# Optimization experiments

Measured on AMD Instinct MI355X. Metric: run time of the kernel, lower is better.

## Reference

```python
import jax, jax.numpy as jnp
import numpy as np

N = 100000   # nodes
DEG = 16     # fixed neighbor count per node
F_IN = 128
F_OUT = 32
H = 4        # heads


def setup_inputs() -> dict:
    key = jax.random.key(0)
    k1, k2, k3, k4 = jax.random.split(key, 4)
    x = jax.random.normal(k1, (N, F_IN), dtype=jnp.float32)
    neigh_idx = jax.random.randint(k2, (N, DEG), 0, N)
    # small scale keeps exp(leaky_relu(score)) well-conditioned (original exp's pre-softmax)
    Ws = jax.random.normal(k3, (H, F_OUT, F_IN), dtype=jnp.float32) * 0.05
    As = jax.random.normal(k4, (H, 2 * F_OUT, 1), dtype=jnp.float32) * 0.05
    return {"x": x, "neigh_idx": neigh_idx, "Ws": Ws, "As": As}


def reference(x, neigh_idx, Ws, As):
    n, _ = x.shape
    h, f_out, _ = Ws.shape
    # transformed node features per head: [H, N, F_out]
    t = jnp.einsum('hoi,ni->hno', Ws, x)
    # score a^T [Wh_src; Wh_dst] decomposes into src + dst dot products
    a = As[..., 0]                      # [H, 2*F_out]
    a_src, a_dst = a[:, :f_out], a[:, f_out:]
    s_src = jnp.einsum('hno,ho->hn', t, a_src)   # [H, N]
    s_dst = jnp.einsum('hno,ho->hn', t, a_dst)   # [H, N]
    # self node goes first in the softmax, matching the original loop
    full_idx = jnp.concatenate([jnp.arange(n)[:, None], neigh_idx], axis=1)  # [N, DEG+1]
    scores = s_src[:, :, None] + s_dst[:, full_idx]                           # [H, N, DEG+1]
    # faithful to original: exp(leaky_relu(.)) THEN softmax (double exponential)
    e = jnp.exp(jax.nn.leaky_relu(scores, 0.2))
    alphas = jax.nn.softmax(e, axis=-1)
    feats = t[:, full_idx]                                                    # [H, N, DEG+1, F_out]
    out = jnp.einsum('hnd,hndf->hnf', alphas, feats)                          # [H, N, F_out]
    # activation 'elu' -> heads concatenated: [N, H*F_out]
    out = jnp.transpose(out, (1, 0, 2)).reshape(n, h * f_out)
    return jax.nn.elu(out)
```

## Files before the change

### kernel.cpp

```cpp
#include <hip/hip_runtime.h>
#include <hip/hip_fp16.h>
#include <math.h>

#define NN 100000
#define DEG 16
#define F_IN 128
#define F_OUT 32
#define NH 4
#define FTOT 128

#define BM 128
#define BK 32
#define PAD 132

__global__ __launch_bounds__(256) void k1_proj(
    const float* __restrict__ x,
    const float* __restrict__ W,
    const float* __restrict__ As,
    __half* __restrict__ t,
    float* __restrict__ ssrc,
    float* __restrict__ sdst) {
    __shared__ float xs[2][BK][PAD];
    __shared__ float ws_[2][BK][PAD];

    const int tid = threadIdx.x;
    const int base = blockIdx.x * BM;

    float4 rx[4], rw[4];

    auto load_chunk = [&](int k0) {
#pragma unroll
        for (int r = 0; r < 4; ++r) {
            const int q = tid + 256 * r;
            const int n = q >> 3;
            const int c = q & 7;
            int ng = base + n;
            if (ng >= NN) ng = NN - 1;
            rx[r] = *(const float4*)(x + (long)ng * F_IN + k0 + 4 * c);
            rw[r] = *(const float4*)(W + n * F_IN + k0 + 4 * c);
        }
    };
    auto write_chunk = [&](int buf) {
#pragma unroll
        for (int r = 0; r < 4; ++r) {
            const int q = tid + 256 * r;
            const int n = q >> 3;
            const int c = q & 7;
            xs[buf][4 * c + 0][n] = rx[r].x;
            xs[buf][4 * c + 1][n] = rx[r].y;
            xs[buf][4 * c + 2][n] = rx[r].z;
            xs[buf][4 * c + 3][n] = rx[r].w;
            ws_[buf][4 * c + 0][n] = rw[r].x;
            ws_[buf][4 * c + 1][n] = rw[r].y;
            ws_[buf][4 * c + 2][n] = rw[r].z;
            ws_[buf][4 * c + 3][n] = rw[r].w;
        }
    };

    load_chunk(0);
    write_chunk(0);
    __syncthreads();
    load_chunk(32);

    const int lane = tid & 63;
    const int wv = tid >> 6;
    const int wr = wv >> 1;
    const int wc = wv & 1;
    const int ln = lane & 7;
    const int lf = lane >> 3;
    const int nq0 = wr * 64 + ln * 8;
    const int fq0 = wc * 64 + lf * 8;

    float acc[8][8];
#pragma unroll
    for (int j = 0; j < 8; ++j)
#pragma unroll
        for (int q = 0; q < 8; ++q) acc[j][q] = 0.f;

    for (int ch = 0; ch < 4; ++ch) {
        const int buf = ch & 1;
#pragma unroll 8
        for (int kk = 0; kk < BK; ++kk) {
            const float4 xa = *(const float4*)&xs[buf][kk][nq0];
            const float4 xb = *(const float4*)&xs[buf][kk][nq0 + 4];
            const float4 wa = *(const float4*)&ws_[buf][kk][fq0];
            const float4 wb = *(const float4*)&ws_[buf][kk][fq0 + 4];
            const float xn[8] = {xa.x, xa.y, xa.z, xa.w, xb.x, xb.y, xb.z, xb.w};
            const float wf[8] = {wa.x, wa.y, wa.z, wa.w, wb.x, wb.y, wb.z, wb.w};
#pragma unroll
            for (int j = 0; j < 8; ++j)
#pragma unroll
                for (int q = 0; q < 8; ++q) acc[j][q] += xn[j] * wf[q];
        }
        if (ch < 3) {
            __syncthreads();
            write_chunk(buf ^ 1);
            __syncthreads();
            if (ch < 2) load_chunk(32 * (ch + 2));
        }
    }

#pragma unroll
    for (int j = 0; j < 8; ++j) {
        const int n = base + nq0 + j;
        if (n < NN) {
            union { __half h[8]; float4 v; } u;
#pragma unroll
            for (int q = 0; q < 8; ++q) u.h[q] = __float2half_rn(acc[j][q]);
            *(float4*)(t + (long)n * FTOT + fq0) = u.v;
        }
    }

    const int h = wc * 2 + (lf >> 2);
    const int o0 = (lf & 3) * 8;
    const float4 a0 = *(const float4*)(As + h * 64 + o0);
    const float4 a1 = *(const float4*)(As + h * 64 + o0 + 4);
    const float4 b0 = *(const float4*)(As + h * 64 + 32 + o0);
    const float4 b1 = *(const float4*)(As + h * 64 + 32 + o0 + 4);
    const float av[8] = {a0.x, a0.y, a0.z, a0.w, a1.x, a1.y, a1.z, a1.w};
    const float bv[8] = {b0.x, b0.y, b0.z, b0.w, b1.x, b1.y, b1.z, b1.w};
#pragma unroll
    for (int j = 0; j < 8; ++j) {
        float ps = 0.f, pd = 0.f;
#pragma unroll
        for (int q = 0; q < 8; ++q) {
            ps += acc[j][q] * av[q];
            pd += acc[j][q] * bv[q];
        }
        ps += __shfl_xor(ps, 8);  ps += __shfl_xor(ps, 16);
        pd += __shfl_xor(pd, 8);  pd += __shfl_xor(pd, 16);
        if ((lf & 3) == 0) {
            const int n = base + nq0 + j;
            if (n < NN) {
                ssrc[(long)n * NH + h] = ps;
                sdst[(long)n * NH + h] = pd;
            }
        }
    }
}

__global__ __launch_bounds__(256) void k2_attn(
    const int* __restrict__ nidx,
    const __half* __restrict__ t,
    const float* __restrict__ ssrc,
    const float* __restrict__ sdst,
    float* __restrict__ out) {
    __shared__ float salpha[4][17][4];
    __shared__ int sidx[4][17];

    const int lane = threadIdx.x & 63;
    const int wv = threadIdx.x >> 6;
    const int n = blockIdx.x * 4 + wv;

    if (lane < 17) {
        sidx[wv][lane] = (lane == 0) ? n : nidx[(long)n * DEG + (lane - 1)];
    }
    __syncthreads();

    unsigned int pre[17];
#pragma unroll
    for (int d = 0; d < 17; ++d) {
        pre[d] = *(const unsigned int*)(t + (long)sidx[wv][d] * FTOT + 2 * lane);
    }

    const int h = lane >> 4;
    const int j = lane & 15;
    const float ssv = ssrc[(long)n * NH + h];

    float e_a;
    {
        float c = ssv + sdst[(long)sidx[wv][j] * NH + h];
        c = fmaxf(c, 0.f) + 0.2f * fminf(c, 0.f);
        e_a = expf(c);
    }
    float e_b = -INFINITY;
    if (j == 15) {
        float c = ssv + sdst[(long)sidx[wv][16] * NH + h];
        c = fmaxf(c, 0.f) + 0.2f * fminf(c, 0.f);
        e_b = expf(c);
    }

    float m = fmaxf(e_a, e_b);
#pragma unroll
    for (int mask = 8; mask >= 1; mask >>= 1)
        m = fmaxf(m, __shfl_xor(m, mask));

    const float pa = expf(e_a - m);
    const float pb = (j == 15) ? expf(e_b - m) : 0.f;
    float s = pa + pb;
#pragma unroll
    for (int mask = 8; mask >= 1; mask >>= 1)
        s += __shfl_xor(s, mask);

    const float inv = 1.0f / s;
    salpha[wv][j][h] = pa * inv;
    if (j == 15) salpha[wv][16][h] = pb * inv;
    __syncthreads();

    const int hc = lane >> 4;
    float ax = 0.f, ay = 0.f;
#pragma unroll
    for (int d = 0; d < 17; ++d) {
        const float a = salpha[wv][d][hc];
        const float2 f = __half22float2(*(const __half2*)&pre[d]);
        ax += a * f.x;
        ay += a * f.y;
    }

    const float yx = ax > 0.f ? ax : expm1f(ax);
    const float yy = ay > 0.f ? ay : expm1f(ay);
    float2 o = make_float2(yx, yy);
    *(float2*)(out + (long)n * FTOT + 2 * lane) = o;
}

extern "C" void kernel_launch(void* const* d_in, const int* in_sizes, int n_in,
                              void* d_out, int out_size, void* d_ws, size_t ws_size,
                              hipStream_t stream) {
    const float* x = (const float*)d_in[0];
    const int* nidx = (const int*)d_in[1];
    const float* W = (const float*)d_in[2];
    const float* As = (const float*)d_in[3];
    float* out = (float*)d_out;

    __half* t = (__half*)d_ws;
    float* ssrc = (float*)((char*)d_ws + (size_t)NN * FTOT * sizeof(__half));
    float* sdst = ssrc + (size_t)NN * NH;

    k1_proj<<<(NN + BM - 1) / BM, 256, 0, stream>>>(x, W, As, t, ssrc, sdst);
    k2_attn<<<NN / 4, 256, 0, stream>>>(nidx, t, ssrc, sdst, out);
}
```

Measured before the change: 219.5 us.

## Rewrite projection GEMM with fp16 MFMA and swizzled LDS; nontemporal loads/stores in attention

The projection kernel drops the fp32 register-tiled FMA GEMM. It converts x and W to fp16 in swizzled shared memory and computes the product with 16x16x32 f16 MFMA instructions, using 64-node tiles. The output tile is staged through LDS for coalesced fp16 stores, and the attention scores are reduced with lane shuffles. The attention kernel switches to nontemporal loads for neighbor indices and nontemporal stores for the output. Rounding x and W to fp16 before the matmul loses input precision, and the whole of W is reloaded per block.

```diff
diff --git a/kernel.cpp b/kernel.cpp
--- a/kernel.cpp
+++ b/kernel.cpp
@@ -9,9 +9,12 @@
 #define NH 4
 #define FTOT 128
 
-#define BM 128
-#define BK 32
-#define PAD 132
+typedef _Float16 f16x8 __attribute__((ext_vector_type(8)));
+typedef float f32x4 __attribute__((ext_vector_type(4)));
+
+__device__ __forceinline__ int swz(int row, int col) {
+    return row * 128 + (col ^ ((row & 7) << 3));
+}
 
 __global__ __launch_bounds__(256) void k1_proj(
     const float* __restrict__ x,
@@ -20,120 +23,114 @@
     __half* __restrict__ t,
     float* __restrict__ ssrc,
     float* __restrict__ sdst) {
-    __shared__ float xs[2][BK][PAD];
-    __shared__ float ws_[2][BK][PAD];
+    __shared__ __half xs[64 * 128];
+    __shared__ __half wsh[128 * 128];
 
     const int tid = threadIdx.x;
-    const int base = blockIdx.x * BM;
-
-    float4 rx[4], rw[4];
-
-    auto load_chunk = [&](int k0) {
-#pragma unroll
-        for (int r = 0; r < 4; ++r) {
-            const int q = tid + 256 * r;
-            const int n = q >> 3;
-            const int c = q & 7;
-            int ng = base + n;
-            if (ng >= NN) ng = NN - 1;
-            rx[r] = *(const float4*)(x + (long)ng * F_IN + k0 + 4 * c);
-            rw[r] = *(const float4*)(W + n * F_IN + k0 + 4 * c);
-        }
-    };
-    auto write_chunk = [&](int buf) {
-#pragma unroll
-        for (int r = 0; r < 4; ++r) {
-            const int q = tid + 256 * r;
-            const int n = q >> 3;
-            const int c = q & 7;
-            xs[buf][4 * c + 0][n] = rx[r].x;
-            xs[buf][4 * c + 1][n] = rx[r].y;
-            xs[buf][4 * c + 2][n] = rx[r].z;
-            xs[buf][4 * c + 3][n] = rx[r].w;
-            ws_[buf][4 * c + 0][n] = rw[r].x;
-            ws_[buf][4 * c + 1][n] = rw[r].y;
-            ws_[buf][4 * c + 2][n] = rw[r].z;
-            ws_[buf][4 * c + 3][n] = rw[r].w;
-        }
-    };
-
-    load_chunk(0);
-    write_chunk(0);
+    const int base = blockIdx.x * 64;
+
+    {
+        const int row = tid >> 2;
+        const int q = tid & 3;
+        int ng = base + row;
+        if (ng >= NN) ng = NN - 1;
+        const float* src = x + (long)ng * F_IN + q * 32;
+#pragma unroll
+        for (int i = 0; i < 4; ++i) {
+            const float4 v0 = *(const float4*)(src + i * 8);
+            const float4 v1 = *(const float4*)(src + i * 8 + 4);
+            union { __half2 h2[4]; float4 f; } u;
+            u.h2[0] = __float22half2_rn(make_float2(v0.x, v0.y));
+            u.h2[1] = __float22half2_rn(make_float2(v0.z, v0.w));
+            u.h2[2] = __float22half2_rn(make_float2(v1.x, v1.y));
+            u.h2[3] = __float22half2_rn(make_float2(v1.z, v1.w));
+            *(float4*)&xs[swz(row, q * 32 + i * 8)] = u.f;
+        }
+    }
+    {
+        const int row = tid >> 1;
+        const int hq = tid & 1;
+        const float* src = W + row * F_IN + hq * 64;
+#pragma unroll
+        for (int i = 0; i < 8; ++i) {
+            const float4 v0 = *(const float4*)(src + i * 8);
+            const float4 v1 = *(const float4*)(src + i * 8 + 4);
+            union { __half2 h2[4]; float4 f; } u;
+            u.h2[0] = __float22half2_rn(make_float2(v0.x, v0.y));
+            u.h2[1] = __float22half2_rn(make_float2(v0.z, v0.w));
+            u.h2[2] = __float22half2_rn(make_float2(v1.x, v1.y));
+            u.h2[3] = __float22half2_rn(make_float2(v1.z, v1.w));
+            *(float4*)&wsh[swz(row, hq * 64 + i * 8)] = u.f;
+        }
+    }
     __syncthreads();
-    load_chunk(32);
 
     const int lane = tid & 63;
     const int wv = tid >> 6;
-    const int wr = wv >> 1;
-    const int wc = wv & 1;
-    const int ln = lane & 7;
-    const int lf = lane >> 3;
-    const int nq0 = wr * 64 + ln * 8;
-    const int fq0 = wc * 64 + lf * 8;
-
-    float acc[8][8];
-#pragma unroll
-    for (int j = 0; j < 8; ++j)
-#pragma unroll
-        for (int q = 0; q < 8; ++q) acc[j][q] = 0.f;
-
-    for (int ch = 0; ch < 4; ++ch) {
-        const int buf = ch & 1;
-#pragma unroll 8
-        for (int kk = 0; kk < BK; ++kk) {
-            const float4 xa = *(const float4*)&xs[buf][kk][nq0];
-            const float4 xb = *(const float4*)&xs[buf][kk][nq0 + 4];
-            const float4 wa = *(const float4*)&ws_[buf][kk][fq0];
-            const float4 wb = *(const float4*)&ws_[buf][kk][fq0 + 4];
-            const float xn[8] = {xa.x, xa.y, xa.z, xa.w, xb.x, xb.y, xb.z, xb.w};
-            const float wf[8] = {wa.x, wa.y, wa.z, wa.w, wb.x, wb.y, wb.z, wb.w};
-#pragma unroll
-            for (int j = 0; j < 8; ++j)
-#pragma unroll
-                for (int q = 0; q < 8; ++q) acc[j][q] += xn[j] * wf[q];
-        }
-        if (ch < 3) {
-            __syncthreads();
-            write_chunk(buf ^ 1);
-            __syncthreads();
-            if (ch < 2) load_chunk(32 * (ch + 2));
-        }
-    }
-
-#pragma unroll
-    for (int j = 0; j < 8; ++j) {
-        const int n = base + nq0 + j;
+    const int mb = wv * 16;
+    const int lr = lane & 15;
+    const int lg = lane >> 4;
+
+    f16x8 afr[4];
+#pragma unroll
+    for (int kk = 0; kk < 4; ++kk)
+        afr[kk] = *(const f16x8*)&xs[swz(mb + lr, kk * 32 + lg * 8)];
+
+    f32x4 acc[8];
+#pragma unroll
+    for (int nt = 0; nt < 8; ++nt) {
+        f32x4 c = {0.f, 0.f, 0.f, 0.f};
+#pragma unroll
+        for (int kk = 0; kk < 4; ++kk) {
+            const f16x8 b =
+                *(const f16x8*)&wsh[swz(nt * 16 + lr, kk * 32 + lg * 8)];
+            c = __builtin_amdgcn_mfma_f32_16x16x32_f16(afr[kk], b, c, 0, 0, 0);
+        }
+        acc[nt] = c;
+    }
+
+    __half* tst = &xs[mb * 128];
+#pragma unroll
+    for (int nt = 0; nt < 8; ++nt) {
+#pragma unroll
+        for (int r = 0; r < 4; ++r) {
+            const int node = lg * 4 + r;
+            const int feat = nt * 16 + lr;
+            tst[node * 128 + (feat ^ ((node & 7) << 3))] =
+                __float2half_rn(acc[nt][r]);
+        }
+    }
+#pragma unroll
+    for (int r = 0; r < 4; ++r) {
+        const int row = r * 4 + lg;
+        const int n = base + mb + row;
         if (n < NN) {
-            union { __half h[8]; float4 v; } u;
-#pragma unroll
-            for (int q = 0; q < 8; ++q) u.h[q] = __float2half_rn(acc[j][q]);
-            *(float4*)(t + (long)n * FTOT + fq0) = u.v;
-        }
-    }
-
-    const int h = wc * 2 + (lf >> 2);
-    const int o0 = (lf & 3) * 8;
-    const float4 a0 = *(const float4*)(As + h * 64 + o0);
-    const float4 a1 = *(const float4*)(As + h * 64 + o0 + 4);
-    const float4 b0 = *(const float4*)(As + h * 64 + 32 + o0);
-    const float4 b1 = *(const float4*)(As + h * 64 + 32 + o0 + 4);
-    const float av[8] = {a0.x, a0.y, a0.z, a0.w, a1.x, a1.y, a1.z, a1.w};
-    const float bv[8] = {b0.x, b0.y, b0.z, b0.w, b1.x, b1.y, b1.z, b1.w};
-#pragma unroll
-    for (int j = 0; j < 8; ++j) {
-        float ps = 0.f, pd = 0.f;
-#pragma unroll
-        for (int q = 0; q < 8; ++q) {
-            ps += acc[j][q] * av[q];
-            pd += acc[j][q] * bv[q];
-        }
-        ps += __shfl_xor(ps, 8);  ps += __shfl_xor(ps, 16);
-        pd += __shfl_xor(pd, 8);  pd += __shfl_xor(pd, 16);
-        if ((lf & 3) == 0) {
-            const int n = base + nq0 + j;
-            if (n < NN) {
-                ssrc[(long)n * NH + h] = ps;
-                sdst[(long)n * NH + h] = pd;
+            const float4 v =
+                *(const float4*)&tst[row * 128 + ((lr * 8) ^ ((row & 7) << 3))];
+            *(float4*)(t + (long)n * FTOT + lr * 8) = v;
+        }
+    }
+
+#pragma unroll
+    for (int h = 0; h < NH; ++h) {
+        const float as0 = As[h * 64 + lr];
+        const float as1 = As[h * 64 + 16 + lr];
+        const float ad0 = As[h * 64 + 32 + lr];
+        const float ad1 = As[h * 64 + 48 + lr];
+#pragma unroll
+        for (int r = 0; r < 4; ++r) {
+            float ps = acc[2 * h][r] * as0 + acc[2 * h + 1][r] * as1;
+            float pd = acc[2 * h][r] * ad0 + acc[2 * h + 1][r] * ad1;
+            ps += __shfl_xor(ps, 1); ps += __shfl_xor(ps, 2);
+            ps += __shfl_xor(ps, 4); ps += __shfl_xor(ps, 8);
+            pd += __shfl_xor(pd, 1); pd += __shfl_xor(pd, 2);
+            pd += __shfl_xor(pd, 4); pd += __shfl_xor(pd, 8);
+            if (lr == 0) {
+                const int n = base + mb + lg * 4 + r;
+                if (n < NN) {
+                    ssrc[(long)n * NH + h] = ps;
+                    sdst[(long)n * NH + h] = pd;
+                }
             }
         }
     }
@@ -153,7 +150,10 @@
     const int n = blockIdx.x * 4 + wv;
 
     if (lane < 17) {
-        sidx[wv][lane] = (lane == 0) ? n : nidx[(long)n * DEG + (lane - 1)];
+        sidx[wv][lane] =
+            (lane == 0)
+                ? n
+                : __builtin_nontemporal_load(&nidx[(long)n * DEG + (lane - 1)]);
     }
     __syncthreads();
 
@@ -209,8 +209,9 @@
 
     const float yx = ax > 0.f ? ax : expm1f(ax);
     const float yy = ay > 0.f ? ay : expm1f(ay);
-    float2 o = make_float2(yx, yy);
-    *(float2*)(out + (long)n * FTOT + 2 * lane) = o;
+    union { float2 f2; double d; } o;
+    o.f2 = make_float2(yx, yy);
+    __builtin_nontemporal_store(o.d, (double*)(out + (long)n * FTOT + 2 * lane));
 }
 
 extern "C" void kernel_launch(void* const* d_in, const int* in_sizes, int n_in,
@@ -226,6 +227,6 @@
     float* ssrc = (float*)((char*)d_ws + (size_t)NN * FTOT * sizeof(__half));
     float* sdst = ssrc + (size_t)NN * NH;
 
-    k1_proj<<<(NN + BM - 1) / BM, 256, 0, stream>>>(x, W, As, t, ssrc, sdst);
+    k1_proj<<<(NN + 63) / 64, 256, 0, stream>>>(x, W, As, t, ssrc, sdst);
     k2_attn<<<NN / 4, 256, 0, stream>>>(nidx, t, ssrc, sdst, out);
 }
```

Measured after the change: 192.1 us. 1.14x faster.
